# Optimization experiments

Measured on AMD Instinct MI355X. Metric: run time of the kernel, lower is better.

Reference implementation:

```python
import jax, jax.numpy as jnp
import numpy as np

D, N = 512, 256          # transition steps, batch
H, L, V = 128, 64, 32000 # h_dim, label_dim, lexicon_size


def _valid_transitions(seed=0):
    # generate a valid shift/reduce schedule: reduce only when stack depth >= 2
    rng = np.random.default_rng(seed)
    ptr = np.zeros(N, np.int64)
    trans = np.zeros((D, N), np.int32)
    for t in range(D):
        r = ((rng.random(N) < 0.6) & (ptr >= 2)).astype(np.int32)
        trans[t] = r
        ptr += 1 - 2 * r  # every step pushes 1; reduce pops 2 first
    return jnp.asarray(trans)


def setup_inputs() -> dict:
    key = jax.random.key(0)
    k1, k2, k3 = jax.random.split(key, 3)
    transitions = _valid_transitions()
    labels_idx = jax.random.randint(k1, (D, N), 0, V, dtype=jnp.int32)
    emb = jax.random.normal(k2, (V, L), jnp.float32) * 0.02
    emb = emb.at[0].set(0.0)  # padding_idx=0
    arg_dim = L + 2 * H
    W = jax.random.normal(k3, (arg_dim, 5 * H), jnp.float32) / np.sqrt(arg_dim).astype(np.float32)
    b = jnp.zeros((5 * H,), jnp.float32)
    leaf = jnp.zeros((H,), jnp.float32)  # leaf_input placeholder vector
    return {"transitions": transitions, "labels_idx": labels_idx,
            "emb": emb, "W": W, "b": b, "leaf": leaf}


def _cell(x, hl, hr, cl, cr, W, b):
    # binary TreeLSTM (Tai et al.): gates from concat(label, h_left, h_right)
    g = jnp.concatenate([x, hl, hr], axis=-1) @ W + b  # [N, 5H]
    i, fl, fr, o, u = jnp.split(g, 5, axis=-1)
    c = jax.nn.sigmoid(i) * jnp.tanh(u) + jax.nn.sigmoid(fl) * cl + jax.nn.sigmoid(fr) * cr
    h = jax.nn.sigmoid(o) * jnp.tanh(c)
    return c, h


def reference(transitions, labels_idx, emb, W, b, leaf):
    labels = emb[labels_idx]  # [D,N,L]
    bidx = jnp.arange(N)

    def step(carry, inp):
        h_st, c_st, idx_st, ptr = carry  # [D,N,H],[D,N,H],[D,N],[N]
        t, mask, lab = inp
        mf = mask.astype(bool)[:, None]
        # right popped first, then left (matches _get_indices call order)
        ridx = idx_st[(ptr - 1) % D, bidx]
        lidx = idx_st[(ptr - 2) % D, bidx]
        hl = jnp.where(mf, h_st[lidx, bidx], leaf)
        hr = jnp.where(mf, h_st[ridx, bidx], leaf)
        cl = jnp.where(mf, c_st[lidx, bidx], leaf)
        cr = jnp.where(mf, c_st[ridx, bidx], leaf)
        c, h = _cell(lab, hl, hr, cl, cr, W, b)
        h_st = h_st.at[t].set(h)   # embeddings_stack[step] = h
        c_st = c_st.at[t].set(c)   # cells_stack[step] = c
        newptr = ptr - 2 * mask    # pops (if reduce)
        idx_st = idx_st.at[newptr, bidx].set(t)  # push current step for all batch
        return (h_st, c_st, idx_st, newptr + 1), None

    h_st = jnp.zeros((D, N, H), jnp.float32)
    c_st = jnp.zeros((D, N, H), jnp.float32)
    idx_st = jnp.zeros((D, N), jnp.int32)
    ptr = jnp.zeros((N,), jnp.int32)
    (h_st, c_st, _, _), _ = jax.lax.scan(
        step, (h_st, c_st, idx_st, ptr),
        (jnp.arange(D, dtype=jnp.int32), transitions, labels))
    # original returns (thin_stack[1][D-1], thin_stack[0][D-1]) = (cells, embeddings)
    return c_st[D - 1], h_st[D - 1]
```

## Files before the change

kernel.cpp:

```cpp
#include <hip/hip_runtime.h>
#include <stdint.h>


#define D     512
#define HD    128
#define LD    64
#define NTHR  512
#define GPR   328

typedef unsigned long long u64t;

__device__ __forceinline__ float sigf(float x){ return 1.0f/(1.0f+__expf(-x)); }
__device__ __forceinline__ float tanh_(float x){ return 1.0f-2.0f/(__expf(2.0f*x)+1.0f); }
__device__ __forceinline__ u64t gld64(const float* p){
  return __hip_atomic_load((const u64t*)p, __ATOMIC_RELAXED, __HIP_MEMORY_SCOPE_AGENT);
}
__device__ __forceinline__ u64t gld64r(const u64t* p){
  return __hip_atomic_load(p, __ATOMIC_RELAXED, __HIP_MEMORY_SCOPE_AGENT);
}
__device__ __forceinline__ void gst32(float* p, float v){
  __hip_atomic_store(p, v, __ATOMIC_RELAXED, __HIP_MEMORY_SCOPE_AGENT);
}
__device__ __forceinline__ void gst64r(u64t* p, u64t v){
  __hip_atomic_store(p, v, __ATOMIC_RELAXED, __HIP_MEMORY_SCOPE_AGENT);
}
__device__ __forceinline__ u64t packw(float v, unsigned tg){
  return ((u64t)tg << 32) | (u64t)__float_as_uint(v);
}
__device__ __forceinline__ float loww(u64t w){
  return __uint_as_float((unsigned)(w & 0xffffffffu));
}

__global__ __launch_bounds__(NTHR,2) void spinn_kernel(
    const int* __restrict__ trans, const int* __restrict__ labels,
    const float* __restrict__ emb, const float* __restrict__ W,
    const float* __restrict__ bias, const float* __restrict__ leaf,
    float* __restrict__ out, u64t* __restrict__ ring,
    float* __restrict__ rec, float* __restrict__ cown)
{
  const int bid = blockIdx.x;
  const int g2 = bid>>1, sl = bid&1, ps = sl^1;
  const int gb0 = g2*2;
  const int tid = threadIdx.x;
  const int kg = tid>>6, lane = tid&63;
  const int cq = lane;

  __shared__ __align__(16) float xs[2][2][320];
  __shared__ __align__(16) float gpq[16][GPR];
  __shared__ float bsl[320];
  __shared__ float lshd[HD];
  __shared__ float clb[2][2][64];
  __shared__ uint8_t mS[D][2];
  __shared__ short liA[D][2];
  __shared__ unsigned short stk_[2][D];

  float4 wr4[40]; float wr1[40];
  {
    const int gq = (cq>>4)*128 + sl*64 + ((cq*4)&63);
    const int gu = 512 + sl*64 + cq;
#pragma unroll
    for (int j=0;j<40;++j){
      int k = kg*40 + j;
      wr4[j] = *(const float4*)(W + (size_t)k*640 + gq);
      wr1[j] = W[(size_t)k*640 + gu];
    }
  }
  if (tid < 320){
    int c = tid;
    int gc = (c < 256) ? ((c>>6)*128 + sl*64 + (c&63)) : (512 + sl*64 + (c-256));
    bsl[c] = bias[gc];
  }
  if (tid < HD) lshd[tid] = leaf[tid];
  if (tid < 2){
    int b = tid, p = 0;
    for (int t=0;t<D;++t){
      int m = trans[t*256 + gb0 + b];
      short li = 0;
      if (m) li = (short)stk_[b][p-2];
      mS[t][b] = (uint8_t)m; liA[t][b] = li;
      int np = p - 2*m; stk_[b][np] = (unsigned short)t; p = np+1;
    }
  }
  __syncthreads();

  for (int idx = tid; idx < 640; idx += NTHR){
    int b = (idx >= 320) ? 1 : 0;
    int r = idx - b*320;
    if (r < 64){
      int row = labels[gb0 + b];
      xs[0][b][r] = emb[(size_t)row*LD + r];
    } else {
      xs[0][b][r] = lshd[(r-64)&127];
    }
  }
  __syncthreads();

  auto gemm = [&](int cur){
    float4 a0 = {0.f,0.f,0.f,0.f}, a1 = {0.f,0.f,0.f,0.f};
    float u0 = 0.f, u1 = 0.f;
#pragma unroll
    for (int j4=0;j4<10;++j4){
      int k = kg*40 + j4*4;
      float4 x0 = *(const float4*)&xs[cur][0][k];
      float4 x1 = *(const float4*)&xs[cur][1][k];
      float xa0[4] = {x0.x,x0.y,x0.z,x0.w};
      float xa1[4] = {x1.x,x1.y,x1.z,x1.w};
#pragma unroll
      for (int jj=0;jj<4;++jj){
        float4 w = wr4[j4*4+jj];
        float wu = wr1[j4*4+jj];
        a0.x = __builtin_fmaf(w.x, xa0[jj], a0.x);
        a0.y = __builtin_fmaf(w.y, xa0[jj], a0.y);
        a0.z = __builtin_fmaf(w.z, xa0[jj], a0.z);
        a0.w = __builtin_fmaf(w.w, xa0[jj], a0.w);
        a1.x = __builtin_fmaf(w.x, xa1[jj], a1.x);
        a1.y = __builtin_fmaf(w.y, xa1[jj], a1.y);
        a1.z = __builtin_fmaf(w.z, xa1[jj], a1.z);
        a1.w = __builtin_fmaf(w.w, xa1[jj], a1.w);
        u0 = __builtin_fmaf(wu, xa0[jj], u0);
        u1 = __builtin_fmaf(wu, xa1[jj], u1);
      }
    }
    *(float4*)&gpq[kg*2+0][cq*4] = a0;
    *(float4*)&gpq[kg*2+1][cq*4] = a1;
    gpq[kg*2+0][256+cq] = u0;
    gpq[kg*2+1][256+cq] = u1;
  };

  float ccprev = 0.f;

  for (int t=0;t<D;++t){
    const int cur = t&1, nxt = cur^1;

    gemm(cur);
    __syncthreads();

    if (tid < 128){
      const int b = tid>>6, dl = tid&63, gd = sl*64+dl;
      const int m = mS[t][b];
      float s[5];
#pragma unroll
      for (int g=0; g<5; ++g){
        int c = (g<4) ? (g*64+dl) : (256+dl);
        float a = 0.f;
#pragma unroll
        for (int kk=0; kk<8; ++kk) a += gpq[kk*2+b][c];
        s[g] = a + bsl[c];
      }
      float cl_ = m ? clb[cur][b][dl] : lshd[gd];
      float cr_ = m ? ccprev : lshd[gd];
      float cc = sigf(s[0])*tanh_(s[4]) + sigf(s[1])*cl_ + sigf(s[2])*cr_;
      float hh = sigf(s[3])*tanh_(cc);
      ccprev = cc;
      gst64r(ring + (((size_t)(t&7)*128 + g2)*2 + sl)*128 + tid,
             packw(hh, (unsigned)(t+1)));
      size_t ro = (((size_t)t*128 + g2)*2 + sl)*128 + b*64 + dl;
      gst32(rec + ro, hh);
      gst32(cown + ro, cc);
      if (t == D-1){
        out[(size_t)(gb0+b)*HD + gd] = cc;
        out[(size_t)256*HD + (size_t)(gb0+b)*HD + gd] = hh;
      } else {
        xs[nxt][b][192+gd] = mS[t+1][b] ? hh : lshd[gd];
      }
      if (t+2 < D && mS[t+2][b] && liA[t+2][b] == t){
        xs[cur][b][64+gd]  = hh;
        clb[cur][b][dl]    = cc;
      }
    } else if (kg == 2){
      if (t+1 < D){
        int b = lane>>5, jj = lane&31;
        int row = labels[(t+1)*256 + gb0 + b];
        float2 ev = *(const float2*)(emb + (size_t)row*LD + jj*2);
        xs[nxt][b][jj*2]   = ev.x;
        xs[nxt][b][jj*2+1] = ev.y;
      }
    } else if (kg == 3){
      if (t+1 < D){
        int b = lane>>5, jj = lane&31;
        int m1 = mS[t+1][b]; int li = liA[t+1][b];
        if (m1){
          if (li <= t-2){
            size_t ro = (((size_t)li*128+g2)*2 + sl)*128 + b*64 + jj*2;
            union{u64t u; float f[2];} h_, c_;
            h_.u = gld64(rec + ro);
            c_.u = gld64(cown + ro);
            xs[nxt][b][64+sl*64+jj*2]   = h_.f[0];
            xs[nxt][b][64+sl*64+jj*2+1] = h_.f[1];
            clb[nxt][b][jj*2]   = c_.f[0];
            clb[nxt][b][jj*2+1] = c_.f[1];
          }
        } else {
          xs[nxt][b][64+sl*64+jj*2]   = lshd[sl*64+jj*2];
          xs[nxt][b][64+sl*64+jj*2+1] = lshd[sl*64+jj*2+1];
          clb[nxt][b][jj*2]   = lshd[sl*64+jj*2];
          clb[nxt][b][jj*2+1] = lshd[sl*64+jj*2+1];
        }
      }
    } else if (kg == 6){
      if (t+1 < D){
        int b = lane>>5, jj = lane&31;
        int m1 = mS[t+1][b]; int li = liA[t+1][b];
        if (m1){
          if (li <= t-2){
            size_t ro = (((size_t)li*128+g2)*2 + ps)*128 + b*64 + jj*2;
            union{u64t u; float f[2];} h_;
            h_.u = gld64(rec + ro);
            xs[nxt][b][64+ps*64+jj*2]   = h_.f[0];
            xs[nxt][b][64+ps*64+jj*2+1] = h_.f[1];
          } else {
            const u64t* rp = ring + (((size_t)((t-1)&7)*128 + g2)*2 + ps)*128
                             + b*64 + jj*2;
            xs[nxt][b][64+ps*64+jj*2]   = loww(gld64r(rp));
            xs[nxt][b][64+ps*64+jj*2+1] = loww(gld64r(rp+1));
          }
        } else {
          xs[nxt][b][64+ps*64+jj*2]   = lshd[ps*64+jj*2];
          xs[nxt][b][64+ps*64+jj*2+1] = lshd[ps*64+jj*2+1];
        }
      }
    } else if (kg == 7){
      if (t+1 < D){
        const u64t* rp = ring + (((size_t)(t&7)*128 + g2)*2 + ps)*128 + lane*2;
        const unsigned want = (unsigned)(t+1);
        u64t w0 = 0, w1 = 0; int it = 0;
        for (;;){
          w0 = gld64r(rp); w1 = gld64r(rp+1);
          int ok = ((unsigned)(w0>>32) == want) & ((unsigned)(w1>>32) == want);
          if (__all(ok)) break;
          __builtin_amdgcn_s_sleep(1);
          if (++it > (1<<20)) break;
        }
        int b = lane>>5, jj = lane&31;
        if (mS[t+1][b]){
          xs[nxt][b][192+ps*64+jj*2]   = loww(w0);
          xs[nxt][b][192+ps*64+jj*2+1] = loww(w1);
        } else {
          xs[nxt][b][192+ps*64+jj*2]   = lshd[ps*64+jj*2];
          xs[nxt][b][192+ps*64+jj*2+1] = lshd[ps*64+jj*2+1];
        }
      }
    }
    __syncthreads();
  }
}

extern "C" void kernel_launch(void* const* d_in, const int* in_sizes, int n_in,
                              void* d_out, int out_size, void* d_ws, size_t ws_size,
                              hipStream_t stream) {
  (void)in_sizes; (void)n_in; (void)out_size; (void)ws_size;
  const int*   trans  = (const int*)d_in[0];
  const int*   labels = (const int*)d_in[1];
  const float* emb    = (const float*)d_in[2];
  const float* W      = (const float*)d_in[3];
  const float* bias   = (const float*)d_in[4];
  const float* leaf   = (const float*)d_in[5];
  float* out = (float*)d_out;

  uint8_t* ws = (uint8_t*)d_ws;
  u64t*  ring = (u64t*)ws;
  float* rec  = (float*)(ws + ((size_t)8<<20));
  float* cown = (float*)(ws + ((size_t)72<<20));

  spinn_kernel<<<dim3(256), dim3(NTHR), 0, stream>>>(
      trans, labels, emb, W, bias, leaf, out, ring, rec, cown);
}
```

Measured before the change: 1.934 ms.

## Overlap partner-block wait with GEMM, split weights between registers and LDS, reduce via LDS atomics

```diff
diff --git a/kernel.cpp b/kernel.cpp
--- a/kernel.cpp
+++ b/kernel.cpp
@@ -6,9 +6,9 @@
 #define HD    128
 #define LD    64
 #define NTHR  512
-#define GPR   328
 
 typedef unsigned long long u64t;
+typedef float f32x2 __attribute__((ext_vector_type(2)));
 
 __device__ __forceinline__ float sigf(float x){ return 1.0f/(1.0f+__expf(-x)); }
 __device__ __forceinline__ float tanh_(float x){ return 1.0f-2.0f/(__expf(2.0f*x)+1.0f); }
@@ -30,6 +30,34 @@
 __device__ __forceinline__ float loww(u64t w){
   return __uint_as_float((unsigned)(w & 0xffffffffu));
 }
+__device__ __forceinline__ int permrow(int k, int sl){
+  const int ps = sl^1;
+  if (k < 64)  return k;
+  if (k < 128) return 64  + sl*64 + (k-64);
+  if (k < 192) return 64  + ps*64 + (k-128);
+  if (k < 256) return 192 + sl*64 + (k-192);
+  return 192 + ps*64 + (k-256);
+}
+
+#define BARRIER() __asm__ volatile("s_waitcnt lgkmcnt(0)\n\ts_barrier" ::: "memory")
+
+#define GEMM4(GETW) { \
+  const float4 x0_ = *(const float4*)&xs[cur][0][kbase]; \
+  const float4 x1_ = *(const float4*)&xs[cur][1][kbase]; \
+  const float xa0_[4] = {x0_.x,x0_.y,x0_.z,x0_.w}; \
+  const float xa1_[4] = {x1_.x,x1_.y,x1_.z,x1_.w}; \
+  _Pragma("unroll") \
+  for (int jj=0;jj<4;++jj){ \
+    f32x2 wA_, wB_; float wu_; GETW; \
+    const f32x2 b0_ = {xa0_[jj], xa0_[jj]}; \
+    const f32x2 b1_ = {xa1_[jj], xa1_[jj]}; \
+    accA0 = __builtin_elementwise_fma(wA_, b0_, accA0); \
+    accB0 = __builtin_elementwise_fma(wB_, b0_, accB0); \
+    u0 = __builtin_fmaf(wu_, xa0_[jj], u0); \
+    accA1 = __builtin_elementwise_fma(wA_, b1_, accA1); \
+    accB1 = __builtin_elementwise_fma(wB_, b1_, accB1); \
+    u1 = __builtin_fmaf(wu_, xa1_[jj], u1); \
+  } }
 
 __global__ __launch_bounds__(NTHR,2) void spinn_kernel(
     const int* __restrict__ trans, const int* __restrict__ labels,
@@ -45,32 +73,46 @@
   const int kg = tid>>6, lane = tid&63;
   const int cq = lane;
 
+  __shared__ __align__(16) float lw[96][320];
   __shared__ __align__(16) float xs[2][2][320];
-  __shared__ __align__(16) float gpq[16][GPR];
+  __shared__ __align__(16) float gpq[2][2][320];
   __shared__ float bsl[320];
   __shared__ float lshd[HD];
   __shared__ float clb[2][2][64];
   __shared__ uint8_t mS[D][2];
   __shared__ short liA[D][2];
   __shared__ unsigned short stk_[2][D];
-
-  float4 wr4[40]; float wr1[40];
+  __shared__ int xflag;
+
+  f32x2 wrA[28], wrB[28]; float wr1[28];
+  const int gq = (cq>>4)*128 + sl*64 + ((cq*4)&63);
+  const int gu = 512 + sl*64 + cq;
   {
-    const int gq = (cq>>4)*128 + sl*64 + ((cq*4)&63);
-    const int gu = 512 + sl*64 + cq;
-#pragma unroll
-    for (int j=0;j<40;++j){
-      int k = kg*40 + j;
-      wr4[j] = *(const float4*)(W + (size_t)k*640 + gq);
-      wr1[j] = W[(size_t)k*640 + gu];
-    }
+#pragma unroll
+    for (int j=0;j<28;++j){
+      const int R = permrow(kg*40+j, sl);
+      const float4 w4 = *(const float4*)(W + (size_t)R*640 + gq);
+      f32x2 a; a.x = w4.x; a.y = w4.y; wrA[j] = a;
+      f32x2 b; b.x = w4.z; b.y = w4.w; wrB[j] = b;
+      wr1[j] = W[(size_t)R*640 + gu];
+    }
+  }
+  for (int idx = tid; idx < 96*320; idx += NTHR){
+    const int r = idx/320, c = idx - r*320;
+    const int kg_ = r/12, m = r - kg_*12;
+    const int R = permrow(kg_*40 + 28 + m, sl);
+    const int gc = (c < 256) ? ((c>>6)*128 + sl*64 + (c&63))
+                             : (512 + sl*64 + (c-256));
+    lw[r][c] = W[(size_t)R*640 + gc];
   }
   if (tid < 320){
-    int c = tid;
-    int gc = (c < 256) ? ((c>>6)*128 + sl*64 + (c&63)) : (512 + sl*64 + (c-256));
+    const int c = tid;
+    const int gc = (c < 256) ? ((c>>6)*128 + sl*64 + (c&63))
+                             : (512 + sl*64 + (c-256));
     bsl[c] = bias[gc];
   }
   if (tid < HD) lshd[tid] = leaf[tid];
+  if (tid == NTHR-1) xflag = 0;
   if (tid < 2){
     int b = tid, p = 0;
     for (int t=0;t<D;++t){
@@ -84,164 +126,189 @@
   __syncthreads();
 
   for (int idx = tid; idx < 640; idx += NTHR){
-    int b = (idx >= 320) ? 1 : 0;
-    int r = idx - b*320;
-    if (r < 64){
-      int row = labels[gb0 + b];
-      xs[0][b][r] = emb[(size_t)row*LD + r];
-    } else {
-      xs[0][b][r] = lshd[(r-64)&127];
-    }
+    const int b = (idx >= 320) ? 1 : 0;
+    const int r = idx - b*320;
+    float v;
+    if (r < 64)       v = emb[(size_t)labels[gb0 + b]*LD + r];
+    else if (r < 128) v = lshd[sl*64 + (r-64)];
+    else if (r < 192) v = lshd[ps*64 + (r-128)];
+    else if (r < 256) v = lshd[sl*64 + (r-192)];
+    else              v = lshd[ps*64 + (r-256)];
+    xs[0][b][r] = v;
+  }
+  for (int c = tid; c < 640; c += NTHR){
+    const int b = (c >= 320) ? 1 : 0;
+    gpq[0][b][c - b*320] = bsl[c - b*320];
   }
   __syncthreads();
-
-  auto gemm = [&](int cur){
-    float4 a0 = {0.f,0.f,0.f,0.f}, a1 = {0.f,0.f,0.f,0.f};
-    float u0 = 0.f, u1 = 0.f;
-#pragma unroll
-    for (int j4=0;j4<10;++j4){
-      int k = kg*40 + j4*4;
-      float4 x0 = *(const float4*)&xs[cur][0][k];
-      float4 x1 = *(const float4*)&xs[cur][1][k];
-      float xa0[4] = {x0.x,x0.y,x0.z,x0.w};
-      float xa1[4] = {x1.x,x1.y,x1.z,x1.w};
-#pragma unroll
-      for (int jj=0;jj<4;++jj){
-        float4 w = wr4[j4*4+jj];
-        float wu = wr1[j4*4+jj];
-        a0.x = __builtin_fmaf(w.x, xa0[jj], a0.x);
-        a0.y = __builtin_fmaf(w.y, xa0[jj], a0.y);
-        a0.z = __builtin_fmaf(w.z, xa0[jj], a0.z);
-        a0.w = __builtin_fmaf(w.w, xa0[jj], a0.w);
-        a1.x = __builtin_fmaf(w.x, xa1[jj], a1.x);
-        a1.y = __builtin_fmaf(w.y, xa1[jj], a1.y);
-        a1.z = __builtin_fmaf(w.z, xa1[jj], a1.z);
-        a1.w = __builtin_fmaf(w.w, xa1[jj], a1.w);
-        u0 = __builtin_fmaf(wu, xa0[jj], u0);
-        u1 = __builtin_fmaf(wu, xa1[jj], u1);
-      }
-    }
-    *(float4*)&gpq[kg*2+0][cq*4] = a0;
-    *(float4*)&gpq[kg*2+1][cq*4] = a1;
-    gpq[kg*2+0][256+cq] = u0;
-    gpq[kg*2+1][256+cq] = u1;
-  };
 
   float ccprev = 0.f;
 
   for (int t=0;t<D;++t){
     const int cur = t&1, nxt = cur^1;
 
-    gemm(cur);
-    __syncthreads();
+    f32x2 accA0 = {0.f,0.f}, accB0 = {0.f,0.f};
+    f32x2 accA1 = {0.f,0.f}, accB1 = {0.f,0.f};
+    float u0 = 0.f, u1 = 0.f;
+
+    if (kg == 7){
+      if (t > 0){
+        const u64t* rp = ring + ((((size_t)((t-1)&7))*128 + g2)*2 + ps)*128 + lane*2;
+        const unsigned want = (unsigned)t;
+        u64t w0 = 0, w1 = 0; int it = 0;
+        for (;;){
+          w0 = gld64r(rp); w1 = gld64r(rp+1);
+          const int ok = ((unsigned)(w0>>32) == want) & ((unsigned)(w1>>32) == want);
+          if (__all(ok)) break;
+          __builtin_amdgcn_s_sleep(1);
+          if (++it > (1<<20)) break;
+        }
+        const int b = lane>>5, jj = lane&31;
+        if (mS[t][b]){
+          xs[cur][b][256+jj*2]   = loww(w0);
+          xs[cur][b][256+jj*2+1] = loww(w1);
+        } else {
+          xs[cur][b][256+jj*2]   = lshd[ps*64+jj*2];
+          xs[cur][b][256+jj*2+1] = lshd[ps*64+jj*2+1];
+        }
+      }
+      __hip_atomic_store(&xflag, t+1, __ATOMIC_RELEASE, __HIP_MEMORY_SCOPE_WORKGROUP);
+    }
+
+#pragma unroll
+    for (int j4=0;j4<4;++j4){
+      const int kbase = kg*40 + j4*4;
+      GEMM4({ wA_ = wrA[j4*4+jj]; wB_ = wrB[j4*4+jj]; wu_ = wr1[j4*4+jj]; });
+    }
+    if (kg == 6){
+      int it = 0;
+      while (__hip_atomic_load(&xflag, __ATOMIC_ACQUIRE, __HIP_MEMORY_SCOPE_WORKGROUP) < t+1){
+        __builtin_amdgcn_s_sleep(1);
+        if (++it > (1<<22)) break;
+      }
+    }
+#pragma unroll
+    for (int j4=4;j4<7;++j4){
+      const int kbase = kg*40 + j4*4;
+      GEMM4({ wA_ = wrA[j4*4+jj]; wB_ = wrB[j4*4+jj]; wu_ = wr1[j4*4+jj]; });
+    }
+#pragma unroll
+    for (int j4=7;j4<10;++j4){
+      const int kbase = kg*40 + j4*4;
+      GEMM4({
+        const int r_ = kg*12 + (j4-7)*4 + jj;
+        const float4 wq_ = *(const float4*)&lw[r_][cq*4];
+        const float wuu_ = lw[r_][256+cq];
+        f32x2 ta_; ta_.x = wq_.x; ta_.y = wq_.y; wA_ = ta_;
+        f32x2 tb_; tb_.x = wq_.z; tb_.y = wq_.w; wB_ = tb_;
+        wu_ = wuu_;
+      });
+    }
+    {
+      float* g0 = &gpq[cur][0][0];
+      float* g1 = &gpq[cur][1][0];
+      __hip_atomic_fetch_add(g0 + cq*4+0, accA0.x, __ATOMIC_RELAXED, __HIP_MEMORY_SCOPE_WORKGROUP);
+      __hip_atomic_fetch_add(g0 + cq*4+1, accA0.y, __ATOMIC_RELAXED, __HIP_MEMORY_SCOPE_WORKGROUP);
+      __hip_atomic_fetch_add(g0 + cq*4+2, accB0.x, __ATOMIC_RELAXED, __HIP_MEMORY_SCOPE_WORKGROUP);
+      __hip_atomic_fetch_add(g0 + cq*4+3, accB0.y, __ATOMIC_RELAXED, __HIP_MEMORY_SCOPE_WORKGROUP);
+      __hip_atomic_fetch_add(g0 + 256+cq,  u0,     __ATOMIC_RELAXED, __HIP_MEMORY_SCOPE_WORKGROUP);
+      __hip_atomic_fetch_add(g1 + cq*4+0, accA1.x, __ATOMIC_RELAXED, __HIP_MEMORY_SCOPE_WORKGROUP);
+      __hip_atomic_fetch_add(g1 + cq*4+1, accA1.y, __ATOMIC_RELAXED, __HIP_MEMORY_SCOPE_WORKGROUP);
+      __hip_atomic_fetch_add(g1 + cq*4+2, accB1.x, __ATOMIC_RELAXED, __HIP_MEMORY_SCOPE_WORKGROUP);
+      __hip_atomic_fetch_add(g1 + cq*4+3, accB1.y, __ATOMIC_RELAXED, __HIP_MEMORY_SCOPE_WORKGROUP);
+      __hip_atomic_fetch_add(g1 + 256+cq,  u1,     __ATOMIC_RELAXED, __HIP_MEMORY_SCOPE_WORKGROUP);
+    }
+    BARRIER();
 
     if (tid < 128){
       const int b = tid>>6, dl = tid&63, gd = sl*64+dl;
       const int m = mS[t][b];
       float s[5];
 #pragma unroll
-      for (int g=0; g<5; ++g){
-        int c = (g<4) ? (g*64+dl) : (256+dl);
-        float a = 0.f;
-#pragma unroll
-        for (int kk=0; kk<8; ++kk) a += gpq[kk*2+b][c];
-        s[g] = a + bsl[c];
-      }
-      float cl_ = m ? clb[cur][b][dl] : lshd[gd];
-      float cr_ = m ? ccprev : lshd[gd];
-      float cc = sigf(s[0])*tanh_(s[4]) + sigf(s[1])*cl_ + sigf(s[2])*cr_;
-      float hh = sigf(s[3])*tanh_(cc);
+      for (int g=0; g<4; ++g) s[g] = gpq[cur][b][g*64+dl];
+      s[4] = gpq[cur][b][256+dl];
+      const float cl_ = m ? clb[cur][b][dl] : lshd[gd];
+      const float cr_ = m ? ccprev : lshd[gd];
+      const float cc = sigf(s[0])*tanh_(s[4]) + sigf(s[1])*cl_ + sigf(s[2])*cr_;
+      const float hh = sigf(s[3])*tanh_(cc);
       ccprev = cc;
       gst64r(ring + (((size_t)(t&7)*128 + g2)*2 + sl)*128 + tid,
              packw(hh, (unsigned)(t+1)));
-      size_t ro = (((size_t)t*128 + g2)*2 + sl)*128 + b*64 + dl;
+      const size_t ro = (((size_t)t*128 + g2)*2 + sl)*128 + b*64 + dl;
       gst32(rec + ro, hh);
       gst32(cown + ro, cc);
       if (t == D-1){
         out[(size_t)(gb0+b)*HD + gd] = cc;
         out[(size_t)256*HD + (size_t)(gb0+b)*HD + gd] = hh;
       } else {
-        xs[nxt][b][192+gd] = mS[t+1][b] ? hh : lshd[gd];
+        xs[nxt][b][192+dl] = mS[t+1][b] ? hh : lshd[gd];
       }
       if (t+2 < D && mS[t+2][b] && liA[t+2][b] == t){
-        xs[cur][b][64+gd]  = hh;
-        clb[cur][b][dl]    = cc;
+        xs[cur][b][64+dl] = hh;
+        clb[cur][b][dl]   = cc;
       }
     } else if (kg == 2){
       if (t+1 < D){
-        int b = lane>>5, jj = lane&31;
-        int row = labels[(t+1)*256 + gb0 + b];
-        float2 ev = *(const float2*)(emb + (size_t)row*LD + jj*2);
+        const int b = lane>>5, jj = lane&31;
+        const int row = labels[(t+1)*256 + gb0 + b];
+        const float2 ev = *(const float2*)(emb + (size_t)row*LD + jj*2);
         xs[nxt][b][jj*2]   = ev.x;
         xs[nxt][b][jj*2+1] = ev.y;
       }
     } else if (kg == 3){
       if (t+1 < D){
-        int b = lane>>5, jj = lane&31;
-        int m1 = mS[t+1][b]; int li = liA[t+1][b];
+        const int b = lane>>5, jj = lane&31;
+        const int m1 = mS[t+1][b]; const int li = liA[t+1][b];
         if (m1){
-          if (li <= t-2){
-            size_t ro = (((size_t)li*128+g2)*2 + sl)*128 + b*64 + jj*2;
+          if (li <= t-1){
+            const size_t ro = (((size_t)li*128+g2)*2 + sl)*128 + b*64 + jj*2;
             union{u64t u; float f[2];} h_, c_;
             h_.u = gld64(rec + ro);
             c_.u = gld64(cown + ro);
-            xs[nxt][b][64+sl*64+jj*2]   = h_.f[0];
-            xs[nxt][b][64+sl*64+jj*2+1] = h_.f[1];
-            clb[nxt][b][jj*2]   = c_.f[0];
-            clb[nxt][b][jj*2+1] = c_.f[1];
+            xs[nxt][b][64+jj*2]   = h_.f[0];
+            xs[nxt][b][64+jj*2+1] = h_.f[1];
+            clb[nxt][b][jj*2]     = c_.f[0];
+            clb[nxt][b][jj*2+1]   = c_.f[1];
           }
         } else {
-          xs[nxt][b][64+sl*64+jj*2]   = lshd[sl*64+jj*2];
-          xs[nxt][b][64+sl*64+jj*2+1] = lshd[sl*64+jj*2+1];
-          clb[nxt][b][jj*2]   = lshd[sl*64+jj*2];
-          clb[nxt][b][jj*2+1] = lshd[sl*64+jj*2+1];
+          xs[nxt][b][64+jj*2]   = lshd[sl*64+jj*2];
+          xs[nxt][b][64+jj*2+1] = lshd[sl*64+jj*2+1];
+          clb[nxt][b][jj*2]     = lshd[sl*64+jj*2];
+          clb[nxt][b][jj*2+1]   = lshd[sl*64+jj*2+1];
         }
       }
-    } else if (kg == 6){
+    } else if (kg == 4){
       if (t+1 < D){
-        int b = lane>>5, jj = lane&31;
-        int m1 = mS[t+1][b]; int li = liA[t+1][b];
+        const int b = lane>>5, jj = lane&31;
+        const int m1 = mS[t+1][b]; const int li = liA[t+1][b];
         if (m1){
           if (li <= t-2){
-            size_t ro = (((size_t)li*128+g2)*2 + ps)*128 + b*64 + jj*2;
+            const size_t ro = (((size_t)li*128+g2)*2 + ps)*128 + b*64 + jj*2;
             union{u64t u; float f[2];} h_;
             h_.u = gld64(rec + ro);
-            xs[nxt][b][64+ps*64+jj*2]   = h_.f[0];
-            xs[nxt][b][64+ps*64+jj*2+1] = h_.f[1];
+            xs[nxt][b][128+jj*2]   = h_.f[0];
+            xs[nxt][b][128+jj*2+1] = h_.f[1];
           } else {
             const u64t* rp = ring + (((size_t)((t-1)&7)*128 + g2)*2 + ps)*128
                              + b*64 + jj*2;
-            xs[nxt][b][64+ps*64+jj*2]   = loww(gld64r(rp));
-            xs[nxt][b][64+ps*64+jj*2+1] = loww(gld64r(rp+1));
+            xs[nxt][b][128+jj*2]   = loww(gld64r(rp));
+            xs[nxt][b][128+jj*2+1] = loww(gld64r(rp+1));
           }
         } else {
-          xs[nxt][b][64+ps*64+jj*2]   = lshd[ps*64+jj*2];
-          xs[nxt][b][64+ps*64+jj*2+1] = lshd[ps*64+jj*2+1];
+          xs[nxt][b][128+jj*2]   = lshd[ps*64+jj*2];
+          xs[nxt][b][128+jj*2+1] = lshd[ps*64+jj*2+1];
         }
       }
-    } else if (kg == 7){
-      if (t+1 < D){
-        const u64t* rp = ring + (((size_t)(t&7)*128 + g2)*2 + ps)*128 + lane*2;
-        const unsigned want = (unsigned)(t+1);
-        u64t w0 = 0, w1 = 0; int it = 0;
-        for (;;){
-          w0 = gld64r(rp); w1 = gld64r(rp+1);
-          int ok = ((unsigned)(w0>>32) == want) & ((unsigned)(w1>>32) == want);
-          if (__all(ok)) break;
-          __builtin_amdgcn_s_sleep(1);
-          if (++it > (1<<20)) break;
-        }
-        int b = lane>>5, jj = lane&31;
-        if (mS[t+1][b]){
-          xs[nxt][b][192+ps*64+jj*2]   = loww(w0);
-          xs[nxt][b][192+ps*64+jj*2+1] = loww(w1);
-        } else {
-          xs[nxt][b][192+ps*64+jj*2]   = lshd[ps*64+jj*2];
-          xs[nxt][b][192+ps*64+jj*2+1] = lshd[ps*64+jj*2+1];
-        }
-      }
-    }
-    __syncthreads();
+    } else if (kg == 5 || kg == 6){
+      const int ii = tid - 320;
+#pragma unroll
+      for (int q=0;q<5;++q){
+        const int c = ii + q*128;
+        const int b = (c >= 320) ? 1 : 0;
+        gpq[nxt][b][c - b*320] = bsl[c - b*320];
+      }
+    }
+    BARRIER();
   }
 }
 
```

Measured after the change: 4.561 ms. 136% more time.

## Overlap peer-block ring wait with GEMM via permuted weight rows

Applied to the files above, without the earlier changes.

```diff
diff --git a/kernel.cpp b/kernel.cpp
--- a/kernel.cpp
+++ b/kernel.cpp
@@ -30,6 +30,16 @@
 __device__ __forceinline__ float loww(u64t w){
   return __uint_as_float((unsigned)(w & 0xffffffffu));
 }
+__device__ __forceinline__ int permrow(int k, int sl){
+  const int ps = sl^1;
+  if (k < 64)  return k;
+  if (k < 128) return 64  + sl*64 + (k-64);
+  if (k < 192) return 64  + ps*64 + (k-128);
+  if (k < 256) return 192 + sl*64 + (k-192);
+  return 192 + ps*64 + (k-256);
+}
+
+#define BARRIER() __asm__ volatile("s_waitcnt lgkmcnt(0)\n\ts_barrier" ::: "memory")
 
 __global__ __launch_bounds__(NTHR,2) void spinn_kernel(
     const int* __restrict__ trans, const int* __restrict__ labels,
@@ -39,7 +49,8 @@
     float* __restrict__ rec, float* __restrict__ cown)
 {
   const int bid = blockIdx.x;
-  const int g2 = bid>>1, sl = bid&1, ps = sl^1;
+  const int g2 = ((bid>>4)<<3) | (bid&7);
+  const int sl = (bid>>3)&1, ps = sl^1;
   const int gb0 = g2*2;
   const int tid = threadIdx.x;
   const int kg = tid>>6, lane = tid&63;
@@ -60,9 +71,9 @@
     const int gu = 512 + sl*64 + cq;
 #pragma unroll
     for (int j=0;j<40;++j){
-      int k = kg*40 + j;
-      wr4[j] = *(const float4*)(W + (size_t)k*640 + gq);
-      wr1[j] = W[(size_t)k*640 + gu];
+      const int R = permrow(kg*40 + j, sl);
+      wr4[j] = *(const float4*)(W + (size_t)R*640 + gq);
+      wr1[j] = W[(size_t)R*640 + gu];
     }
   }
   if (tid < 320){
@@ -84,22 +95,22 @@
   __syncthreads();
 
   for (int idx = tid; idx < 640; idx += NTHR){
-    int b = (idx >= 320) ? 1 : 0;
-    int r = idx - b*320;
-    if (r < 64){
-      int row = labels[gb0 + b];
-      xs[0][b][r] = emb[(size_t)row*LD + r];
-    } else {
-      xs[0][b][r] = lshd[(r-64)&127];
-    }
+    const int b = (idx >= 320) ? 1 : 0;
+    const int r = idx - b*320;
+    float v;
+    if (r < 64)       v = emb[(size_t)labels[gb0 + b]*LD + r];
+    else if (r < 128) v = lshd[sl*64 + (r-64)];
+    else if (r < 192) v = lshd[ps*64 + (r-128)];
+    else if (r < 256) v = lshd[sl*64 + (r-192)];
+    else              v = lshd[ps*64 + (r-256)];
+    xs[0][b][r] = v;
   }
   __syncthreads();
 
-  auto gemm = [&](int cur){
-    float4 a0 = {0.f,0.f,0.f,0.f}, a1 = {0.f,0.f,0.f,0.f};
-    float u0 = 0.f, u1 = 0.f;
-#pragma unroll
-    for (int j4=0;j4<10;++j4){
+  auto gemmr = [&](int cur, int j0, int j1,
+                   float4& a0, float4& a1, float& u0, float& u1){
+#pragma unroll
+    for (int j4=j0;j4<j1;++j4){
       int k = kg*40 + j4*4;
       float4 x0 = *(const float4*)&xs[cur][0][k];
       float4 x1 = *(const float4*)&xs[cur][1][k];
@@ -121,10 +132,6 @@
         u1 = __builtin_fmaf(wu, xa1[jj], u1);
       }
     }
-    *(float4*)&gpq[kg*2+0][cq*4] = a0;
-    *(float4*)&gpq[kg*2+1][cq*4] = a1;
-    gpq[kg*2+0][256+cq] = u0;
-    gpq[kg*2+1][256+cq] = u1;
   };
 
   float ccprev = 0.f;
@@ -132,8 +139,59 @@
   for (int t=0;t<D;++t){
     const int cur = t&1, nxt = cur^1;
 
-    gemm(cur);
-    __syncthreads();
+    {
+      float4 a0 = {0.f,0.f,0.f,0.f}, a1 = {0.f,0.f,0.f,0.f};
+      float u0 = 0.f, u1 = 0.f;
+
+      if (kg <= 5){
+        gemmr(cur, 0, 10, a0, a1, u0, u1);
+      } else if (kg == 6){
+        gemmr(cur, 0, 4, a0, a1, u0, u1);
+        if (t > 0){
+          const size_t rb = ((((size_t)((t-1)&7))*128 + g2)*2 + ps)*128;
+          const unsigned want = (unsigned)t;
+          const bool act = (lane < 24) || (lane >= 32 && lane < 56);
+          const int b = lane >> 5;
+          const int dl = act ? (b ? lane-32 : lane) : 0;
+          const u64t* rp = ring + rb + b*64 + dl;
+          u64t w0 = ((u64t)want)<<32; int it = 0;
+          for (;;){
+            if (act) w0 = gld64r(rp);
+            if (__all((unsigned)(w0>>32) == want)) break;
+            if (++it > (1<<20)) break;
+          }
+          if (act)
+            xs[cur][b][256+dl] = mS[t][b] ? loww(w0) : lshd[ps*64+dl];
+        }
+        gemmr(cur, 4, 10, a0, a1, u0, u1);
+      } else {
+        if (t > 0){
+          const size_t rb = ((((size_t)((t-1)&7))*128 + g2)*2 + ps)*128;
+          const unsigned want = (unsigned)t;
+          const bool act = (lane < 40);
+          const int dl = 24 + (act ? lane : 0);
+          const u64t* rp0 = ring + rb + dl;
+          const u64t* rp1 = ring + rb + 64 + dl;
+          u64t w0 = ((u64t)want)<<32, w1 = w0; int it = 0;
+          for (;;){
+            if (act){ w0 = gld64r(rp0); w1 = gld64r(rp1); }
+            if (__all(((unsigned)(w0>>32) == want) &
+                      ((unsigned)(w1>>32) == want))) break;
+            if (++it > (1<<20)) break;
+          }
+          if (act){
+            xs[cur][0][256+dl] = mS[t][0] ? loww(w0) : lshd[ps*64+dl];
+            xs[cur][1][256+dl] = mS[t][1] ? loww(w1) : lshd[ps*64+dl];
+          }
+        }
+        gemmr(cur, 0, 10, a0, a1, u0, u1);
+      }
+      *(float4*)&gpq[kg*2+0][cq*4] = a0;
+      *(float4*)&gpq[kg*2+1][cq*4] = a1;
+      gpq[kg*2+0][256+cq] = u0;
+      gpq[kg*2+1][256+cq] = u1;
+    }
+    BARRIER();
 
     if (tid < 128){
       const int b = tid>>6, dl = tid&63, gd = sl*64+dl;
@@ -147,101 +205,80 @@
         for (int kk=0; kk<8; ++kk) a += gpq[kk*2+b][c];
         s[g] = a + bsl[c];
       }
-      float cl_ = m ? clb[cur][b][dl] : lshd[gd];
-      float cr_ = m ? ccprev : lshd[gd];
-      float cc = sigf(s[0])*tanh_(s[4]) + sigf(s[1])*cl_ + sigf(s[2])*cr_;
-      float hh = sigf(s[3])*tanh_(cc);
+      const float cl_ = m ? clb[cur][b][dl] : lshd[gd];
+      const float cr_ = m ? ccprev : lshd[gd];
+      const float cc = sigf(s[0])*tanh_(s[4]) + sigf(s[1])*cl_ + sigf(s[2])*cr_;
+      const float hh = sigf(s[3])*tanh_(cc);
       ccprev = cc;
       gst64r(ring + (((size_t)(t&7)*128 + g2)*2 + sl)*128 + tid,
              packw(hh, (unsigned)(t+1)));
-      size_t ro = (((size_t)t*128 + g2)*2 + sl)*128 + b*64 + dl;
+      const size_t ro = (((size_t)t*128 + g2)*2 + sl)*128 + b*64 + dl;
       gst32(rec + ro, hh);
       gst32(cown + ro, cc);
       if (t == D-1){
         out[(size_t)(gb0+b)*HD + gd] = cc;
         out[(size_t)256*HD + (size_t)(gb0+b)*HD + gd] = hh;
       } else {
-        xs[nxt][b][192+gd] = mS[t+1][b] ? hh : lshd[gd];
+        xs[nxt][b][192+dl] = mS[t+1][b] ? hh : lshd[gd];
       }
       if (t+2 < D && mS[t+2][b] && liA[t+2][b] == t){
-        xs[cur][b][64+gd]  = hh;
-        clb[cur][b][dl]    = cc;
+        xs[cur][b][64+dl] = hh;
+        clb[cur][b][dl]   = cc;
       }
     } else if (kg == 2){
       if (t+1 < D){
-        int b = lane>>5, jj = lane&31;
-        int row = labels[(t+1)*256 + gb0 + b];
-        float2 ev = *(const float2*)(emb + (size_t)row*LD + jj*2);
+        const int b = lane>>5, jj = lane&31;
+        const int row = labels[(t+1)*256 + gb0 + b];
+        const float2 ev = *(const float2*)(emb + (size_t)row*LD + jj*2);
         xs[nxt][b][jj*2]   = ev.x;
         xs[nxt][b][jj*2+1] = ev.y;
       }
     } else if (kg == 3){
       if (t+1 < D){
-        int b = lane>>5, jj = lane&31;
-        int m1 = mS[t+1][b]; int li = liA[t+1][b];
+        const int b = lane>>5, jj = lane&31;
+        const int m1 = mS[t+1][b]; const int li = liA[t+1][b];
         if (m1){
           if (li <= t-2){
-            size_t ro = (((size_t)li*128+g2)*2 + sl)*128 + b*64 + jj*2;
+            const size_t ro = (((size_t)li*128+g2)*2 + sl)*128 + b*64 + jj*2;
             union{u64t u; float f[2];} h_, c_;
             h_.u = gld64(rec + ro);
             c_.u = gld64(cown + ro);
-            xs[nxt][b][64+sl*64+jj*2]   = h_.f[0];
-            xs[nxt][b][64+sl*64+jj*2+1] = h_.f[1];
-            clb[nxt][b][jj*2]   = c_.f[0];
-            clb[nxt][b][jj*2+1] = c_.f[1];
+            xs[nxt][b][64+jj*2]   = h_.f[0];
+            xs[nxt][b][64+jj*2+1] = h_.f[1];
+            clb[nxt][b][jj*2]     = c_.f[0];
+            clb[nxt][b][jj*2+1]   = c_.f[1];
           }
         } else {
-          xs[nxt][b][64+sl*64+jj*2]   = lshd[sl*64+jj*2];
-          xs[nxt][b][64+sl*64+jj*2+1] = lshd[sl*64+jj*2+1];
-          clb[nxt][b][jj*2]   = lshd[sl*64+jj*2];
-          clb[nxt][b][jj*2+1] = lshd[sl*64+jj*2+1];
+          xs[nxt][b][64+jj*2]   = lshd[sl*64+jj*2];
+          xs[nxt][b][64+jj*2+1] = lshd[sl*64+jj*2+1];
+          clb[nxt][b][jj*2]     = lshd[sl*64+jj*2];
+          clb[nxt][b][jj*2+1]   = lshd[sl*64+jj*2+1];
         }
       }
-    } else if (kg == 6){
+    } else if (kg == 4){
       if (t+1 < D){
-        int b = lane>>5, jj = lane&31;
-        int m1 = mS[t+1][b]; int li = liA[t+1][b];
+        const int b = lane>>5, jj = lane&31;
+        const int m1 = mS[t+1][b]; const int li = liA[t+1][b];
         if (m1){
           if (li <= t-2){
-            size_t ro = (((size_t)li*128+g2)*2 + ps)*128 + b*64 + jj*2;
+            const size_t ro = (((size_t)li*128+g2)*2 + ps)*128 + b*64 + jj*2;
             union{u64t u; float f[2];} h_;
             h_.u = gld64(rec + ro);
-            xs[nxt][b][64+ps*64+jj*2]   = h_.f[0];
-            xs[nxt][b][64+ps*64+jj*2+1] = h_.f[1];
+            xs[nxt][b][128+jj*2]   = h_.f[0];
+            xs[nxt][b][128+jj*2+1] = h_.f[1];
           } else {
             const u64t* rp = ring + (((size_t)((t-1)&7)*128 + g2)*2 + ps)*128
                              + b*64 + jj*2;
-            xs[nxt][b][64+ps*64+jj*2]   = loww(gld64r(rp));
-            xs[nxt][b][64+ps*64+jj*2+1] = loww(gld64r(rp+1));
+            xs[nxt][b][128+jj*2]   = loww(gld64r(rp));
+            xs[nxt][b][128+jj*2+1] = loww(gld64r(rp+1));
           }
         } else {
-          xs[nxt][b][64+ps*64+jj*2]   = lshd[ps*64+jj*2];
-          xs[nxt][b][64+ps*64+jj*2+1] = lshd[ps*64+jj*2+1];
+          xs[nxt][b][128+jj*2]   = lshd[ps*64+jj*2];
+          xs[nxt][b][128+jj*2+1] = lshd[ps*64+jj*2+1];
         }
       }
-    } else if (kg == 7){
-      if (t+1 < D){
-        const u64t* rp = ring + (((size_t)(t&7)*128 + g2)*2 + ps)*128 + lane*2;
-        const unsigned want = (unsigned)(t+1);
-        u64t w0 = 0, w1 = 0; int it = 0;
-        for (;;){
-          w0 = gld64r(rp); w1 = gld64r(rp+1);
-          int ok = ((unsigned)(w0>>32) == want) & ((unsigned)(w1>>32) == want);
-          if (__all(ok)) break;
-          __builtin_amdgcn_s_sleep(1);
-          if (++it > (1<<20)) break;
-        }
-        int b = lane>>5, jj = lane&31;
-        if (mS[t+1][b]){
-          xs[nxt][b][192+ps*64+jj*2]   = loww(w0);
-          xs[nxt][b][192+ps*64+jj*2+1] = loww(w1);
-        } else {
-          xs[nxt][b][192+ps*64+jj*2]   = lshd[ps*64+jj*2];
-          xs[nxt][b][192+ps*64+jj*2+1] = lshd[ps*64+jj*2+1];
-        }
-      }
-    }
-    __syncthreads();
+    }
+    BARRIER();
   }
 }
 
```

Measured after the change: 2.224 ms. 15.0% more time.
